# Kernel tuning notes

Hardware: AMD Instinct MI355X
Metric: run time of the kernel (lower is better)

The kernel has to match this reference:

```python
import jax, jax.numpy as jnp
import numpy as np

HEADS = 8
LN_EPS = 1e-5
BN_EPS = 1e-5
MIN_EPS, MAX_EPS = 1e-4, 10.0


def _ln(x, g, b):
    m = x.mean(-1, keepdims=True)
    v = x.var(-1, keepdims=True)
    return (x - m) / jnp.sqrt(v + LN_EPS) * g + b


def _pos2d(a, b, dim, temperature=10000.0):
    # faithful to build_2d_sincos_position_embedding(w=a, h=b)
    grid_a = jnp.arange(a, dtype=jnp.float32)
    grid_b = jnp.arange(b, dtype=jnp.float32)
    ga, gb = jnp.meshgrid(grid_a, grid_b, indexing='ij')  # (a, b)
    pos_dim = dim // 4
    omega = 1.0 / (temperature ** (jnp.arange(pos_dim, dtype=jnp.float32) / pos_dim))
    out_a = ga.flatten()[:, None] * omega[None]
    out_b = gb.flatten()[:, None] * omega[None]
    return jnp.concatenate([jnp.sin(out_a), jnp.cos(out_a), jnp.sin(out_b), jnp.cos(out_b)], axis=1)  # (a*b, dim)


def _avgpool(x, k):
    bb, cc, H, W = x.shape
    return x.reshape(bb, cc, H // k, k, W // k, k).mean((3, 5))


def setup_inputs() -> dict:
    key = jax.random.key(0)
    c1, c2, bs = 256, 512, 16
    ks = jax.random.split(key, 12)

    def lin(k, o, i):
        return (jax.random.normal(k, (o, i), jnp.float32) * (1.0 / np.sqrt(i))).astype(jnp.float32)

    return {
        'a3': jax.random.normal(ks[0], (bs, c1, 80, 80), jnp.float32),
        'a4': jax.random.normal(ks[1], (bs, c2, 40, 40), jnp.float32),
        'conv_w': lin(ks[2], c1, c2), 'conv_b': jnp.zeros((c1,), jnp.float32),
        'bn_g': jnp.ones((c1,), jnp.float32), 'bn_b': jnp.zeros((c1,), jnp.float32),
        'q_w': lin(ks[3], c1, c1), 'q_b': jnp.zeros((c1,), jnp.float32),
        'q_ln_g': jnp.ones((c1,), jnp.float32), 'q_ln_b': jnp.zeros((c1,), jnp.float32),
        'k_w': lin(ks[4], c1, c1), 'k_b': jnp.zeros((c1,), jnp.float32),
        'k_ln_g': jnp.ones((c1,), jnp.float32), 'k_ln_b': jnp.zeros((c1,), jnp.float32),
        'v_w': lin(ks[5], c1, c1), 'v_b': jnp.zeros((c1,), jnp.float32),
        'out_w': lin(ks[6], c1, c1), 'out_b': jnp.zeros((c1,), jnp.float32),
        'lin1_w': lin(ks[7], 4 * c1, c1), 'lin1_b': jnp.zeros((4 * c1,), jnp.float32),
        'lin2_w': lin(ks[8], c1, 4 * c1), 'lin2_b': jnp.zeros((c1,), jnp.float32),
        'norm1_g': jnp.ones((c1,), jnp.float32), 'norm1_b': jnp.zeros((c1,), jnp.float32),
        'norm2_g': jnp.ones((c1,), jnp.float32), 'norm2_b': jnp.zeros((c1,), jnp.float32),
        'idx': 10,
    }


def reference(a3, a4, conv_w, conv_b, bn_g, bn_b, q_w, q_b, q_ln_g, q_ln_b,
              k_w, k_b, k_ln_g, k_ln_b, v_w, v_b, out_w, out_b,
              lin1_w, lin1_b, lin2_w, lin2_b, norm1_g, norm1_b, norm2_g, norm2_b, idx):
    a3 = jnp.nan_to_num(a3, nan=0.0, posinf=1e4, neginf=-1e4)
    a4 = jnp.nan_to_num(a4, nan=0.0, posinf=1e4, neginf=-1e4)
    orig_a3, orig_a4 = a3, a4

    # high_to_low_embed: 1x1 conv + BatchNorm (eval: running_mean=0, running_var=1)
    a4e = jnp.einsum('bchw,oc->bohw', a4, conv_w) + conv_b[None, :, None, None]
    a4e = a4e / jnp.sqrt(1.0 + BN_EPS) * bn_g[None, :, None, None] + bn_b[None, :, None, None]

    if idx == 10:
        a3d = _avgpool(a3, 2)
    else:
        a3d = _avgpool(a3, 4)
        a4e = _avgpool(a4e, 2)

    bs, c, h, w = a3d.shape
    tgt = h * w
    src = a4e.shape[2] * a4e.shape[3]

    residual = a3d.reshape(bs, c, tgt).transpose(0, 2, 1)      # (bs, tgt, c)
    a3f = a3d.reshape(bs, c, tgt).transpose(2, 0, 1)            # (tgt, bs, c)
    a4f = a4e.reshape(bs, c, src).transpose(2, 0, 1)            # (src, bs, c)

    pos = _pos2d(h, w, c)[:, None, :]                           # (h*w, 1, c)
    a3f = a3f + pos
    a4f = a4f + pos                                             # src == tgt by construction

    Q = jax.nn.relu(_ln(a3f @ q_w.T + q_b, q_ln_g, q_ln_b))
    K = jax.nn.relu(_ln(a4f @ k_w.T + k_b, k_ln_g, k_ln_b))
    V = a4f @ v_w.T + v_b

    hd = c // HEADS
    Q = Q.reshape(tgt, bs, HEADS, hd).transpose(1, 2, 0, 3)     # (b, h, tgt, hd)
    K = K.reshape(src, bs, HEADS, hd).transpose(1, 2, 0, 3)
    V = V.reshape(src, bs, HEADS, hd).transpose(1, 2, 0, 3)

    m = max(src, tgt)
    wi = (np.pi / 2) * jnp.arange(1, m + 1, dtype=jnp.float32) / m  # (m,)
    sq = jnp.sin(wi[:tgt])[None, None, :, None]
    cq = jnp.cos(wi[:tgt])[None, None, :, None]
    sk = jnp.sin(wi[:src])[None, None, :, None]
    ck = jnp.cos(wi[:src])[None, None, :, None]
    Q_ = jnp.concatenate([Q * sq, Q * cq], -1)                  # (b, h, tgt, 2hd)
    K_ = jnp.concatenate([K * sk, K * ck], -1)                  # (b, h, src, 2hd)

    KV = jnp.einsum('bhsd,bhse->bhde', K_, V)                   # (b, h, 2hd, hd)
    Zden = jnp.einsum('bhld,bhd->bhl', Q_, K_.sum(2))
    Z = 1.0 / jnp.clip(Zden, MIN_EPS, MAX_EPS)
    attn = jnp.einsum('bhld,bhde->bhle', Q_, KV) * Z[..., None]  # (b, h, tgt, hd)

    attn = attn.transpose(2, 0, 1, 3).reshape(tgt, bs, c)
    out = (attn @ out_w.T + out_b).transpose(1, 0, 2)           # (bs, tgt, c)
    out = _ln(out, norm1_g, norm1_b)
    out = residual + out

    res2 = out
    ff = jax.nn.gelu(out @ lin1_w.T + lin1_b, approximate=False) @ lin2_w.T + lin2_b
    ff = _ln(ff, norm2_g, norm2_b)
    out = res2 + ff

    a3_sa = out.transpose(0, 2, 1).reshape(bs, c, h, w)
    a3_sa = jax.image.resize(a3_sa, orig_a3.shape, 'bilinear')  # align_corners=False
    a3_sa = a3_sa * orig_a3

    B4, C4, H4, W4 = orig_a4.shape
    a4_up = jax.image.resize(orig_a4, (B4, C4, 2 * H4, 2 * W4), 'bilinear')
    return (a3_sa, a4_up)
```

## Files before the change

### kernel.cpp

```cpp
#include <hip/hip_runtime.h>
#include <math.h>


typedef __attribute__((ext_vector_type(8))) short bf16x8;
typedef __attribute__((ext_vector_type(8))) unsigned short us8;
typedef __attribute__((ext_vector_type(4))) unsigned short us4h;
typedef __attribute__((ext_vector_type(4))) float f32x4;

__device__ __forceinline__ unsigned short f2bf(float f) {
  unsigned int u = __float_as_uint(f);
  u += 0x7fff + ((u >> 16) & 1);
  return (unsigned short)(u >> 16);
}
__device__ __forceinline__ float bf2f(unsigned short u) {
  return __uint_as_float(((unsigned int)u) << 16);
}

__device__ __forceinline__ void gload16(const void* g, void* l) {
  __builtin_amdgcn_global_load_lds(
      (const __attribute__((address_space(1))) void*)g,
      (__attribute__((address_space(3))) void*)l, 16, 0, 0);
}

__global__ __launch_bounds__(256) void wprep_kernel(
    const float* __restrict__ cw, const float* __restrict__ qw,
    const float* __restrict__ kw, const float* __restrict__ vw,
    const float* __restrict__ ow, const float* __restrict__ l1w,
    const float* __restrict__ l2w, unsigned short* __restrict__ wbf) {
  int gid = blockIdx.x * 256 + threadIdx.x;
  size_t e0 = (size_t)gid * 8;
  const float* src; size_t off;
  if (e0 < 131072)      { src = cw;  off = e0; }
  else if (e0 < 196608) { src = qw;  off = e0 - 131072; }
  else if (e0 < 262144) { src = kw;  off = e0 - 196608; }
  else if (e0 < 327680) { src = vw;  off = e0 - 262144; }
  else if (e0 < 393216) { src = ow;  off = e0 - 327680; }
  else if (e0 < 655360) { src = l1w; off = e0 - 393216; }
  else                  { src = l2w; off = e0 - 655360; }
  float4 v0 = *(const float4*)(src + off);
  float4 v1 = *(const float4*)(src + off + 4);
  us8 r;
  r[0] = f2bf(v0.x); r[1] = f2bf(v0.y); r[2] = f2bf(v0.z); r[3] = f2bf(v0.w);
  r[4] = f2bf(v1.x); r[5] = f2bf(v1.y); r[6] = f2bf(v1.z); r[7] = f2bf(v1.w);
  *(us8*)(wbf + e0) = r;
}

__global__ void pos_kernel(float* __restrict__ pos) {
  int s = blockIdx.x, c = threadIdx.x;
  int y = s / 40, x = s - y * 40;
  int quad = c >> 6, i = c & 63;
  float omega = expf(-(float)i * (9.2103403719761836f / 64.0f));
  float coord = (quad < 2) ? (float)y : (float)x;
  float a = coord * omega;
  pos[s * 256 + c] = (quad & 1) ? cosf(a) : sinf(a);
}

__global__ __launch_bounds__(640) void avgpool_kernel(
    const float* __restrict__ a3, const float* __restrict__ pos,
    unsigned short* __restrict__ X3) {
  __shared__ float buf2[256][44];
  int y = blockIdx.x, b = blockIdx.y;
  int tid = threadIdx.x;
  int x2 = tid % 20, cq = tid / 20;
#pragma unroll
  for (int it = 0; it < 8; ++it) {
    int c = cq + 32 * it;
    const float* p = a3 + (((size_t)(b * 256 + c) * 80 + 2 * y) * 80 + x2 * 4);
    float4 r0 = *(const float4*)p;
    float4 r1 = *(const float4*)(p + 80);
    buf2[c][2 * x2]     = 0.25f * ((r0.x + r0.y) + (r1.x + r1.y));
    buf2[c][2 * x2 + 1] = 0.25f * ((r0.z + r0.w) + (r1.z + r1.w));
  }
  __syncthreads();
  size_t t0 = (size_t)b * 1600 + y * 40;
  int sbase = y * 40;
#pragma unroll
  for (int it = 0; it < 4; ++it) {
    int idx = it * 640 + tid;
    int c = idx & 255, xq = idx >> 8;
    int x0 = xq * 4;
    float4 v = *(const float4*)&buf2[c][x0];
#pragma unroll
    for (int j = 0; j < 4; ++j) {
      float pv = pos[(size_t)(sbase + x0 + j) * 256 + c];
      float vv = (j == 0) ? v.x : (j == 1) ? v.y : (j == 2) ? v.z : v.w;
      X3[(t0 + x0 + j) * 256 + c] = f2bf(vv + pv);
    }
  }
}

__global__ __launch_bounds__(256) void a4t_kernel(
    const float* __restrict__ a4, unsigned short* __restrict__ a4t) {
  __shared__ float buf[64][65];
  int s0 = blockIdx.x * 64, k0 = blockIdx.y * 64, b = blockIdx.z;
  const float* src = a4 + ((size_t)b * 512 + k0) * 1600 + s0;
#pragma unroll
  for (int p = 0; p < 4; ++p) {
    int idx = p * 256 + threadIdx.x;
    int kk = idx >> 4, s4 = (idx & 15) * 4;
    float4 v = *(const float4*)(src + (size_t)kk * 1600 + s4);
    buf[kk][s4 + 0] = v.x; buf[kk][s4 + 1] = v.y;
    buf[kk][s4 + 2] = v.z; buf[kk][s4 + 3] = v.w;
  }
  __syncthreads();
  unsigned short* dst = a4t + ((size_t)b * 1600 + s0) * 512 + k0;
#pragma unroll
  for (int p = 0; p < 4; ++p) {
    int idx = p * 256 + threadIdx.x;
    int ss = idx >> 4, kq = (idx & 15) * 4;
    us4h v;
    v[0] = f2bf(buf[kq + 0][ss]); v[1] = f2bf(buf[kq + 1][ss]);
    v[2] = f2bf(buf[kq + 2][ss]); v[3] = f2bf(buf[kq + 3][ss]);
    *(us4h*)(dst + (size_t)ss * 512 + kq) = v;
  }
}

struct __align__(16) SmemT {
  unsigned short Albs[64][32];
  unsigned short Wlds[256][32];
  float part[4][64][2];
};

template<int EPI>
__device__ __forceinline__ void gemm_body(
    SmemT& S,
    const unsigned short* __restrict__ A, const unsigned short* __restrict__ W,
    const float* __restrict__ bias, void* __restrict__ outp,
    const int K, const int ldN, int t0, int o0,
    const float* __restrict__ posb,
    const float* __restrict__ g1, const float* __restrict__ b1,
    const unsigned short* __restrict__ res) {
  int tid = threadIdx.x;
  int lane = tid & 63, w = tid >> 6;
  int g = lane >> 4, cl = lane & 15;
  int n0 = w * 64;
  f32x4 acc[4][4] = {};

  int arow = lane >> 2, acol = (lane & 3) * 8;
  const unsigned short* ag  = A + (size_t)(t0 + w * 16 + arow) * K + acol;
  const unsigned short* wg0 = W + (size_t)(o0 + (w)      * 16 + arow) * K + acol;
  const unsigned short* wg1 = W + (size_t)(o0 + (4 + w)  * 16 + arow) * K + acol;
  const unsigned short* wg2 = W + (size_t)(o0 + (8 + w)  * 16 + arow) * K + acol;
  const unsigned short* wg3 = W + (size_t)(o0 + (12 + w) * 16 + arow) * K + acol;
  unsigned short* al  = &S.Albs[w * 16][0];
  unsigned short* wl0 = &S.Wlds[(w) * 16][0];
  unsigned short* wl1 = &S.Wlds[(4 + w) * 16][0];
  unsigned short* wl2 = &S.Wlds[(8 + w) * 16][0];
  unsigned short* wl3 = &S.Wlds[(12 + w) * 16][0];

  for (int k0 = 0; k0 < K; k0 += 32) {
    __syncthreads();
    gload16(ag + k0, al);
    gload16(wg0 + k0, wl0);
    gload16(wg1 + k0, wl1);
    gload16(wg2 + k0, wl2);
    gload16(wg3 + k0, wl3);
    __syncthreads();
    bf16x8 af[4], bw[4];
#pragma unroll
    for (int ms = 0; ms < 4; ++ms)
      af[ms] = *(const bf16x8*)&S.Albs[ms * 16 + cl][g * 8];
#pragma unroll
    for (int ns = 0; ns < 4; ++ns)
      bw[ns] = *(const bf16x8*)&S.Wlds[n0 + ns * 16 + cl][g * 8];
#pragma unroll
    for (int ms = 0; ms < 4; ++ms)
#pragma unroll
      for (int ns = 0; ns < 4; ++ns)
        acc[ms][ns] = __builtin_amdgcn_mfma_f32_16x16x32_bf16(af[ms], bw[ns], acc[ms][ns], 0, 0, 0);
  }

  float bv[4];
#pragma unroll
  for (int ns = 0; ns < 4; ++ns) bv[ns] = bias[o0 + n0 + ns * 16 + cl];
  int sbase = t0 % 1600;

  if constexpr (EPI == 2 || EPI == 3 || EPI == 5) {
#pragma unroll
    for (int ms = 0; ms < 4; ++ms) {
#pragma unroll
      for (int i = 0; i < 4; ++i) {
        float p = 0.f, q = 0.f;
#pragma unroll
        for (int ns = 0; ns < 4; ++ns) {
          float v = acc[ms][ns][i] + bv[ns];
          p += v; q += v * v;
        }
        p += __shfl_xor(p, 1); q += __shfl_xor(q, 1);
        p += __shfl_xor(p, 2); q += __shfl_xor(q, 2);
        p += __shfl_xor(p, 4); q += __shfl_xor(q, 4);
        p += __shfl_xor(p, 8); q += __shfl_xor(q, 8);
        if (cl == 0) {
          int rl = ms * 16 + g * 4 + i;
          S.part[w][rl][0] = p;
          S.part[w][rl][1] = q;
        }
      }
    }
    __syncthreads();
  }

  if constexpr (EPI == 5) {
    float* of = (float*)outp;
    int bb = t0 / 1600;
#pragma unroll
    for (int ms = 0; ms < 4; ++ms) {
      int rl0 = ms * 16 + g * 4;
      float mean[4], inv[4];
#pragma unroll
      for (int i = 0; i < 4; ++i) {
        float sp = (S.part[0][rl0 + i][0] + S.part[1][rl0 + i][0]) +
                   (S.part[2][rl0 + i][0] + S.part[3][rl0 + i][0]);
        float sq = (S.part[0][rl0 + i][1] + S.part[1][rl0 + i][1]) +
                   (S.part[2][rl0 + i][1] + S.part[3][rl0 + i][1]);
        mean[i] = sp * (1.f / 256.f);
        float var = sq * (1.f / 256.f) - mean[i] * mean[i];
        inv[i] = rsqrtf(var + 1e-5f);
      }
#pragma unroll
      for (int ns = 0; ns < 4; ++ns) {
        int col = n0 + ns * 16 + cl;
        float gg = g1[col], b2 = b1[col];
        float4 y;
#pragma unroll
        for (int i = 0; i < 4; ++i) {
          float v = acc[ms][ns][i] + bv[ns];
          float yy = (v - mean[i]) * inv[i] * gg + b2;
          yy += bf2f(res[(size_t)(t0 + rl0 + i) * 256 + col]);
          if (i == 0) y.x = yy; else if (i == 1) y.y = yy;
          else if (i == 2) y.z = yy; else y.w = yy;
        }
        *(float4*)(of + ((size_t)(bb * 256 + col) * 1600) + sbase + rl0) = y;
      }
    }
    return;
  }

  unsigned short* ob = (unsigned short*)outp;
#pragma unroll
  for (int ms = 0; ms < 4; ++ms) {
#pragma unroll
    for (int i = 0; i < 4; ++i) {
      int rl = ms * 16 + g * 4 + i;
      int t = t0 + rl;
      float mean = 0.f, inv = 0.f;
      if constexpr (EPI == 2 || EPI == 3) {
        float sp = (S.part[0][rl][0] + S.part[1][rl][0]) + (S.part[2][rl][0] + S.part[3][rl][0]);
        float sq = (S.part[0][rl][1] + S.part[1][rl][1]) + (S.part[2][rl][1] + S.part[3][rl][1]);
        mean = sp * (1.f / 256.f);
        float var = sq * (1.f / 256.f) - mean * mean;
        inv = rsqrtf(var + 1e-5f);
      }
#pragma unroll
      for (int ns = 0; ns < 4; ++ns) {
        int col = n0 + ns * 16 + cl;
        float v = acc[ms][ns][i] + bv[ns];
        size_t oidx = (size_t)t * ldN + o0 + col;
        if constexpr (EPI == 0) {
          ob[oidx] = f2bf(v);
        } else if constexpr (EPI == 1) {
          const float is = 0.99999500003749968f;
          float y = v * (is * g1[col]) + b1[col] + posb[(size_t)(sbase + rl) * 256 + col];
          ob[oidx] = f2bf(y);
        } else if constexpr (EPI == 2) {
          float y = (v - mean) * inv * g1[col] + b1[col];
          ob[oidx] = f2bf(fmaxf(y, 0.f));
        } else if constexpr (EPI == 3) {
          float y = (v - mean) * inv * g1[col] + b1[col];
          y += bf2f(res[(size_t)t * 256 + col]) - posb[(size_t)(sbase + rl) * 256 + col];
          ob[oidx] = f2bf(y);
        } else if constexpr (EPI == 4) {
          float y = 0.5f * v * (1.f + erff(v * 0.7071067811865475f));
          ob[oidx] = f2bf(y);
        }
      }
    }
  }
}

template<int EPI>
__global__ __launch_bounds__(256) void fgemm(
    const unsigned short* __restrict__ A, const unsigned short* __restrict__ W,
    const float* __restrict__ bias, void* __restrict__ outp,
    const int K, const int ldN,
    const float* __restrict__ posb,
    const float* __restrict__ g1, const float* __restrict__ b1,
    const unsigned short* __restrict__ res) {
  __shared__ SmemT S;
  gemm_body<EPI>(S, A, W, bias, outp, K, ldN, blockIdx.x * 64, blockIdx.y * 256,
                 posb, g1, b1, res);
}

__global__ __launch_bounds__(256) void qkv_kernel(
    const unsigned short* __restrict__ X3b, const unsigned short* __restrict__ X4b,
    const unsigned short* __restrict__ w_q, const unsigned short* __restrict__ w_k,
    const unsigned short* __restrict__ w_v,
    const float* __restrict__ q_b, const float* __restrict__ k_b, const float* __restrict__ v_b,
    const float* __restrict__ q_g, const float* __restrict__ q_bt,
    const float* __restrict__ k_g, const float* __restrict__ k_bt,
    unsigned short* __restrict__ Qo, unsigned short* __restrict__ Ko,
    unsigned short* __restrict__ Vo) {
  __shared__ SmemT S;
  int t0 = blockIdx.x * 64;
  if (blockIdx.y == 0) {
    gemm_body<2>(S, X3b, w_q, q_b, Qo, 256, 256, t0, 0, nullptr, q_g, q_bt, nullptr);
  } else if (blockIdx.y == 1) {
    gemm_body<2>(S, X4b, w_k, k_b, Ko, 256, 256, t0, 0, nullptr, k_g, k_bt, nullptr);
  } else {
    gemm_body<0>(S, X4b, w_v, v_b, Vo, 256, 256, t0, 0, nullptr, nullptr, nullptr, nullptr);
  }
}

__global__ __launch_bounds__(256) void kv_kernel(
    const unsigned short* __restrict__ Kb, const unsigned short* __restrict__ Vb,
    float* __restrict__ KVp, float* __restrict__ Ksp) {
  __shared__ float Kc[64][32];
  __shared__ float Vc[64][32];
  __shared__ float sv[64], cv[64];
  __shared__ float red[4][64];
  int bx = blockIdx.x;
  int bh = bx / 5, sp = bx - bh * 5;
  int b = bh >> 3, h = bh & 7;
  int tid = threadIdx.x;
  int e = tid & 31, dg = tid >> 5;
  int d4 = dg * 4;
  int dks = tid & 63, partid = tid >> 6;
  float accs[4] = {0.f, 0.f, 0.f, 0.f};
  float accc[4] = {0.f, 0.f, 0.f, 0.f};
  float ks = 0.f;
  size_t base = ((size_t)b * 1600) * 256 + h * 32;
  for (int s0 = sp * 320; s0 < sp * 320 + 320; s0 += 64) {
    __syncthreads();
#pragma unroll
    for (int p = 0; p < 8; ++p) {
      int si = dg + p * 8;
      Kc[si][e] = bf2f(Kb[base + (size_t)(s0 + si) * 256 + e]);
      Vc[si][e] = bf2f(Vb[base + (size_t)(s0 + si) * 256 + e]);
    }
    if (tid < 64) {
      float wv = 1.5707963267948966f * (float)(s0 + tid + 1) * (1.0f / 1600.0f);
      sv[tid] = sinf(wv);
      cv[tid] = cosf(wv);
    }
    __syncthreads();
#pragma unroll 8
    for (int si = 0; si < 64; ++si) {
      float vv = Vc[si][e];
      float sn = sv[si], cs = cv[si];
      float4 k4 = *(const float4*)&Kc[si][d4];
      float p0 = k4.x * vv, p1 = k4.y * vv, p2 = k4.z * vv, p3 = k4.w * vv;
      accs[0] = fmaf(p0, sn, accs[0]); accc[0] = fmaf(p0, cs, accc[0]);
      accs[1] = fmaf(p1, sn, accs[1]); accc[1] = fmaf(p1, cs, accc[1]);
      accs[2] = fmaf(p2, sn, accs[2]); accc[2] = fmaf(p2, cs, accc[2]);
      accs[3] = fmaf(p3, sn, accs[3]); accc[3] = fmaf(p3, cs, accc[3]);
    }
#pragma unroll 4
    for (int q = 0; q < 16; ++q) {
      int si = partid * 16 + q;
      float kvv = (dks < 32) ? Kc[si][dks] * sv[si] : Kc[si][dks - 32] * cv[si];
      ks += kvv;
    }
  }
  red[partid][dks] = ks;
  __syncthreads();
  size_t ob = (size_t)sp * 128 + bh;
  if (tid < 64)
    Ksp[ob * 64 + tid] = (red[0][tid] + red[1][tid]) + (red[2][tid] + red[3][tid]);
#pragma unroll
  for (int i = 0; i < 4; ++i) {
    KVp[ob * 2048 + (d4 + i) * 32 + e] = accs[i];
    KVp[ob * 2048 + (32 + d4 + i) * 32 + e] = accc[i];
  }
}

__global__ __launch_bounds__(256) void kvred_kernel(
    const float* __restrict__ KVp, const float* __restrict__ Ksp,
    float* __restrict__ KV, float* __restrict__ Ks) {
  int bh = blockIdx.x, tid = threadIdx.x;
  size_t o = (size_t)bh * 2048 + tid * 8;
  float4 s0 = make_float4(0, 0, 0, 0), s1 = make_float4(0, 0, 0, 0);
#pragma unroll
  for (int sp = 0; sp < 5; ++sp) {
    const float* p = KVp + ((size_t)sp * 128 + bh) * 2048 + tid * 8;
    float4 a = *(const float4*)p;
    float4 b2 = *(const float4*)(p + 4);
    s0.x += a.x; s0.y += a.y; s0.z += a.z; s0.w += a.w;
    s1.x += b2.x; s1.y += b2.y; s1.z += b2.z; s1.w += b2.w;
  }
  *(float4*)(KV + o) = s0;
  *(float4*)(KV + o + 4) = s1;
  if (tid < 64) {
    float t = 0.f;
#pragma unroll
    for (int sp = 0; sp < 5; ++sp) t += Ksp[((size_t)sp * 128 + bh) * 64 + tid];
    Ks[bh * 64 + tid] = t;
  }
}

__global__ __launch_bounds__(256) void attn_kernel(
    const unsigned short* __restrict__ Qb, const float* __restrict__ KV,
    const float* __restrict__ Ksum, unsigned short* __restrict__ attn) {
  int grp = threadIdx.x >> 5;
  int e = threadIdx.x & 31;
  int t = blockIdx.x * 8 + grp;
  int b = t / 1600, s = t - b * 1600;
  float wv = 1.5707963267948966f * (float)(s + 1) * (1.0f / 1600.0f);
  float sq = sinf(wv), cq = cosf(wv);
  const unsigned short* qrow = Qb + (size_t)t * 256;
  for (int h = 0; h < 8; ++h) {
    int bh = b * 8 + h;
    const float* kv = KV + (size_t)bh * 2048;
    const float* ksm = Ksum + (size_t)bh * 64;
    float qe = bf2f(qrow[h * 32 + e]);
    float zp = qe * (sq * ksm[e] + cq * ksm[32 + e]);
    zp += __shfl_xor(zp, 1); zp += __shfl_xor(zp, 2);
    zp += __shfl_xor(zp, 4); zp += __shfl_xor(zp, 8); zp += __shfl_xor(zp, 16);
    float acc = 0.f;
#pragma unroll 8
    for (int d = 0; d < 32; ++d) {
      float qv = bf2f(qrow[h * 32 + d]);
      acc = fmaf(qv * sq, kv[d * 32 + e], acc);
      acc = fmaf(qv * cq, kv[(32 + d) * 32 + e], acc);
    }
    float zc = fminf(fmaxf(zp, 1e-4f), 10.0f);
    attn[(size_t)t * 256 + h * 32 + e] = f2bf(acc * (1.0f / zc));
  }
}

__device__ __forceinline__ float4 up_row4(const float* sm, int Y, int q) {
  float fy = Y * 0.5f - 0.25f;
  int iy = (int)floorf(fy);
  float dy = fy - (float)iy;
  int y0 = iy < 0 ? 0 : iy;
  int y1 = (iy + 1) > 39 ? 39 : (iy + 1);
  const float* r0 = sm + y0 * 40;
  const float* r1 = sm + y1 * 40;
  int cm1 = (2 * q - 1) < 0 ? 0 : (2 * q - 1);
  int cp2 = (2 * q + 2) > 39 ? 39 : (2 * q + 2);
  float w1 = 1.f - dy;
  float s0 = w1 * r0[cm1]       + dy * r1[cm1];
  float s1 = w1 * r0[2 * q]     + dy * r1[2 * q];
  float s2 = w1 * r0[2 * q + 1] + dy * r1[2 * q + 1];
  float s3 = w1 * r0[cp2]       + dy * r1[cp2];
  float4 o;
  o.x = 0.25f * s0 + 0.75f * s1;
  o.y = 0.75f * s1 + 0.25f * s2;
  o.z = 0.25f * s1 + 0.75f * s2;
  o.w = 0.75f * s2 + 0.25f * s3;
  return o;
}

__global__ __launch_bounds__(256) void upsample_fused_kernel(
    const float* __restrict__ a3p, const float* __restrict__ a3,
    const float* __restrict__ a4, float* __restrict__ out0,
    float* __restrict__ out1) {
  __shared__ float sm[1600];
  int id = blockIdx.x;
  const float* src;
  float* outp;
  const float* mul = nullptr;
  if (id < 4096) {
    int c = id & 255, b = id >> 8;
    src = a3p + ((size_t)b * 256 + c) * 1600;
    outp = out0 + ((size_t)b * 256 + c) * 6400;
    mul = a3 + ((size_t)b * 256 + c) * 6400;
  } else {
    int id2 = id - 4096;
    int c = id2 & 511, b = id2 >> 9;
    src = a4 + ((size_t)b * 512 + c) * 1600;
    outp = out1 + ((size_t)b * 512 + c) * 6400;
  }
  for (int i = threadIdx.x; i < 400; i += 256)
    *(float4*)&sm[i * 4] = *(const float4*)(src + i * 4);
  __syncthreads();
  if (mul) {
    for (int i = threadIdx.x; i < 1600; i += 256) {
      int Y = i / 20, q = i - Y * 20;
      float4 o = up_row4(sm, Y, q);
      float4 m = *(const float4*)(mul + i * 4);
      o.x *= m.x; o.y *= m.y; o.z *= m.z; o.w *= m.w;
      *(float4*)(outp + i * 4) = o;
    }
  } else {
    for (int i = threadIdx.x; i < 1600; i += 256) {
      int Y = i / 20, q = i - Y * 20;
      float4 o = up_row4(sm, Y, q);
      *(float4*)(outp + i * 4) = o;
    }
  }
}

extern "C" void kernel_launch(void* const* d_in, const int* in_sizes, int n_in,
                              void* d_out, int out_size, void* d_ws, size_t ws_size,
                              hipStream_t stream) {
  const float* a3     = (const float*)d_in[0];
  const float* a4     = (const float*)d_in[1];
  const float* conv_w = (const float*)d_in[2];
  const float* conv_b = (const float*)d_in[3];
  const float* bn_g   = (const float*)d_in[4];
  const float* bn_b   = (const float*)d_in[5];
  const float* q_w    = (const float*)d_in[6];
  const float* q_b    = (const float*)d_in[7];
  const float* q_ln_g = (const float*)d_in[8];
  const float* q_ln_b = (const float*)d_in[9];
  const float* k_w    = (const float*)d_in[10];
  const float* k_b    = (const float*)d_in[11];
  const float* k_ln_g = (const float*)d_in[12];
  const float* k_ln_b = (const float*)d_in[13];
  const float* v_w    = (const float*)d_in[14];
  const float* v_b    = (const float*)d_in[15];
  const float* out_w  = (const float*)d_in[16];
  const float* out_b  = (const float*)d_in[17];
  const float* lin1_w = (const float*)d_in[18];
  const float* lin1_b = (const float*)d_in[19];
  const float* lin2_w = (const float*)d_in[20];
  const float* lin2_b = (const float*)d_in[21];
  const float* n1_g   = (const float*)d_in[22];
  const float* n1_b   = (const float*)d_in[23];
  const float* n2_g   = (const float*)d_in[24];
  const float* n2_b   = (const float*)d_in[25];
  (void)in_sizes; (void)n_in; (void)out_size; (void)ws_size;

  float* ws = (float*)d_ws;
  float* pos  = ws + 0;
  unsigned short* wbf = (unsigned short*)(ws + 409600);
  float* KV   = ws + 868352;
  float* Ks   = ws + 1130496;
  float* KVp  = ws + 1138688;
  float* Ksp  = ws + 2449408;
  unsigned short* X3b  = (unsigned short*)(ws + 2490368);
  unsigned short* X4b  = (unsigned short*)(ws + 5767168);
  unsigned short* Qbb  = (unsigned short*)(ws + 9043968);
  unsigned short* Kbb  = (unsigned short*)(ws + 12320768);
  unsigned short* Vbb  = (unsigned short*)(ws + 15597568);
  unsigned short* o1b  = (unsigned short*)(ws + 18874368);
  unsigned short* a4tb = (unsigned short*)(ws + 22151168);
  unsigned short* ffhb = (unsigned short*)(ws + 22151168);
  float* a3p  = ws + 9043968;

  const unsigned short* w_conv = wbf;
  const unsigned short* w_q    = wbf + 131072;
  const unsigned short* w_k    = wbf + 196608;
  const unsigned short* w_v    = wbf + 262144;
  const unsigned short* w_o    = wbf + 327680;
  const unsigned short* w_l1   = wbf + 393216;
  const unsigned short* w_l2   = wbf + 655360;

  float* out0 = (float*)d_out;
  float* out1f = out0 + (size_t)16 * 256 * 80 * 80;

  wprep_kernel<<<448, 256, 0, stream>>>(conv_w, q_w, k_w, v_w, out_w, lin1_w, lin2_w, wbf);
  pos_kernel<<<1600, 256, 0, stream>>>(pos);
  avgpool_kernel<<<dim3(40, 16), 640, 0, stream>>>(a3, pos, X3b);
  a4t_kernel<<<dim3(25, 8, 16), 256, 0, stream>>>(a4, a4tb);
  fgemm<1><<<dim3(400, 1), 256, 0, stream>>>(a4tb, w_conv, conv_b, X4b, 512, 256, pos, bn_g, bn_b, nullptr);
  qkv_kernel<<<dim3(400, 3), 256, 0, stream>>>(X3b, X4b, w_q, w_k, w_v,
      q_b, k_b, v_b, q_ln_g, q_ln_b, k_ln_g, k_ln_b, Qbb, Kbb, Vbb);
  kv_kernel<<<640, 256, 0, stream>>>(Kbb, Vbb, KVp, Ksp);
  kvred_kernel<<<128, 256, 0, stream>>>(KVp, Ksp, KV, Ks);
  attn_kernel<<<3200, 256, 0, stream>>>(Qbb, KV, Ks, Kbb );
  fgemm<3><<<dim3(400, 1), 256, 0, stream>>>(Kbb, w_o, out_b, o1b, 256, 256, pos, n1_g, n1_b, X3b);
  fgemm<4><<<dim3(400, 4), 256, 0, stream>>>(o1b, w_l1, lin1_b, ffhb, 256, 1024, nullptr, nullptr, nullptr, nullptr);
  fgemm<5><<<dim3(400, 1), 256, 0, stream>>>(ffhb, w_l2, lin2_b, a3p, 1024, 256, nullptr, n2_g, n2_b, o1b);
  upsample_fused_kernel<<<12288, 256, 0, stream>>>(a3p, a3, a4, out0, out1f);
}
```

Before: 417.2 us.

## Use 8-wave GEMM blocks with 2x4 warp tiling and merge prep kernels

The shared GEMM body now runs 8 waves per block instead of 4. Waves form a 2x4 grid, each computing a 32x64 subtile rather than 64x256/4, which halves per-wave accumulators and shares the LDS loading across more waves. The aim is more latency hiding and lower register pressure per wave, at the cost of larger blocks and more barrier participants. The weight-conversion and positional-embedding kernels are merged into one launch to save a kernel launch.

```diff
diff --git a/kernel.cpp b/kernel.cpp
--- a/kernel.cpp
+++ b/kernel.cpp
@@ -22,37 +22,38 @@
       (__attribute__((address_space(3))) void*)l, 16, 0, 0);
 }
 
-__global__ __launch_bounds__(256) void wprep_kernel(
+__global__ __launch_bounds__(256) void prep_kernel(
     const float* __restrict__ cw, const float* __restrict__ qw,
     const float* __restrict__ kw, const float* __restrict__ vw,
     const float* __restrict__ ow, const float* __restrict__ l1w,
-    const float* __restrict__ l2w, unsigned short* __restrict__ wbf) {
-  int gid = blockIdx.x * 256 + threadIdx.x;
-  size_t e0 = (size_t)gid * 8;
-  const float* src; size_t off;
-  if (e0 < 131072)      { src = cw;  off = e0; }
-  else if (e0 < 196608) { src = qw;  off = e0 - 131072; }
-  else if (e0 < 262144) { src = kw;  off = e0 - 196608; }
-  else if (e0 < 327680) { src = vw;  off = e0 - 262144; }
-  else if (e0 < 393216) { src = ow;  off = e0 - 327680; }
-  else if (e0 < 655360) { src = l1w; off = e0 - 393216; }
-  else                  { src = l2w; off = e0 - 655360; }
-  float4 v0 = *(const float4*)(src + off);
-  float4 v1 = *(const float4*)(src + off + 4);
-  us8 r;
-  r[0] = f2bf(v0.x); r[1] = f2bf(v0.y); r[2] = f2bf(v0.z); r[3] = f2bf(v0.w);
-  r[4] = f2bf(v1.x); r[5] = f2bf(v1.y); r[6] = f2bf(v1.z); r[7] = f2bf(v1.w);
-  *(us8*)(wbf + e0) = r;
-}
-
-__global__ void pos_kernel(float* __restrict__ pos) {
-  int s = blockIdx.x, c = threadIdx.x;
-  int y = s / 40, x = s - y * 40;
-  int quad = c >> 6, i = c & 63;
-  float omega = expf(-(float)i * (9.2103403719761836f / 64.0f));
-  float coord = (quad < 2) ? (float)y : (float)x;
-  float a = coord * omega;
-  pos[s * 256 + c] = (quad & 1) ? cosf(a) : sinf(a);
+    const float* __restrict__ l2w, unsigned short* __restrict__ wbf,
+    float* __restrict__ pos) {
+  if (blockIdx.x < 448) {
+    int gid = blockIdx.x * 256 + threadIdx.x;
+    size_t e0 = (size_t)gid * 8;
+    const float* src; size_t off;
+    if (e0 < 131072)      { src = cw;  off = e0; }
+    else if (e0 < 196608) { src = qw;  off = e0 - 131072; }
+    else if (e0 < 262144) { src = kw;  off = e0 - 196608; }
+    else if (e0 < 327680) { src = vw;  off = e0 - 262144; }
+    else if (e0 < 393216) { src = ow;  off = e0 - 327680; }
+    else if (e0 < 655360) { src = l1w; off = e0 - 393216; }
+    else                  { src = l2w; off = e0 - 655360; }
+    float4 v0 = *(const float4*)(src + off);
+    float4 v1 = *(const float4*)(src + off + 4);
+    us8 r;
+    r[0] = f2bf(v0.x); r[1] = f2bf(v0.y); r[2] = f2bf(v0.z); r[3] = f2bf(v0.w);
+    r[4] = f2bf(v1.x); r[5] = f2bf(v1.y); r[6] = f2bf(v1.z); r[7] = f2bf(v1.w);
+    *(us8*)(wbf + e0) = r;
+  } else {
+    int s = blockIdx.x - 448, c = threadIdx.x;
+    int y = s / 40, x = s - y * 40;
+    int quad = c >> 6, i = c & 63;
+    float omega = expf(-(float)i * (9.2103403719761836f / 64.0f));
+    float coord = (quad < 2) ? (float)y : (float)x;
+    float a = coord * omega;
+    pos[s * 256 + c] = (quad & 1) ? cosf(a) : sinf(a);
+  }
 }
 
 __global__ __launch_bounds__(640) void avgpool_kernel(
@@ -132,39 +133,33 @@
     const unsigned short* __restrict__ res) {
   int tid = threadIdx.x;
   int lane = tid & 63, w = tid >> 6;
+  int mw = w >> 2, nw = w & 3;
   int g = lane >> 4, cl = lane & 15;
-  int n0 = w * 64;
-  f32x4 acc[4][4] = {};
+  f32x4 acc[2][4] = {};
 
   int arow = lane >> 2, acol = (lane & 3) * 8;
-  const unsigned short* ag  = A + (size_t)(t0 + w * 16 + arow) * K + acol;
-  const unsigned short* wg0 = W + (size_t)(o0 + (w)      * 16 + arow) * K + acol;
-  const unsigned short* wg1 = W + (size_t)(o0 + (4 + w)  * 16 + arow) * K + acol;
-  const unsigned short* wg2 = W + (size_t)(o0 + (8 + w)  * 16 + arow) * K + acol;
-  const unsigned short* wg3 = W + (size_t)(o0 + (12 + w) * 16 + arow) * K + acol;
-  unsigned short* al  = &S.Albs[w * 16][0];
-  unsigned short* wl0 = &S.Wlds[(w) * 16][0];
-  unsigned short* wl1 = &S.Wlds[(4 + w) * 16][0];
-  unsigned short* wl2 = &S.Wlds[(8 + w) * 16][0];
-  unsigned short* wl3 = &S.Wlds[(12 + w) * 16][0];
+  const unsigned short* ag  = A + (size_t)(t0 + (w & 3) * 16 + arow) * K + acol;
+  const unsigned short* wgA = W + (size_t)(o0 + w * 16 + arow) * K + acol;
+  const unsigned short* wgB = W + (size_t)(o0 + 128 + w * 16 + arow) * K + acol;
+  unsigned short* al  = &S.Albs[(w & 3) * 16][0];
+  unsigned short* wlA = &S.Wlds[w * 16][0];
+  unsigned short* wlB = &S.Wlds[128 + w * 16][0];
 
   for (int k0 = 0; k0 < K; k0 += 32) {
     __syncthreads();
-    gload16(ag + k0, al);
-    gload16(wg0 + k0, wl0);
-    gload16(wg1 + k0, wl1);
-    gload16(wg2 + k0, wl2);
-    gload16(wg3 + k0, wl3);
+    if (w < 4) gload16(ag + k0, al);
+    gload16(wgA + k0, wlA);
+    gload16(wgB + k0, wlB);
     __syncthreads();
-    bf16x8 af[4], bw[4];
-#pragma unroll
-    for (int ms = 0; ms < 4; ++ms)
-      af[ms] = *(const bf16x8*)&S.Albs[ms * 16 + cl][g * 8];
+    bf16x8 af[2], bw[4];
+#pragma unroll
+    for (int ms = 0; ms < 2; ++ms)
+      af[ms] = *(const bf16x8*)&S.Albs[mw * 32 + ms * 16 + cl][g * 8];
 #pragma unroll
     for (int ns = 0; ns < 4; ++ns)
-      bw[ns] = *(const bf16x8*)&S.Wlds[n0 + ns * 16 + cl][g * 8];
-#pragma unroll
-    for (int ms = 0; ms < 4; ++ms)
+      bw[ns] = *(const bf16x8*)&S.Wlds[nw * 64 + ns * 16 + cl][g * 8];
+#pragma unroll
+    for (int ms = 0; ms < 2; ++ms)
 #pragma unroll
       for (int ns = 0; ns < 4; ++ns)
         acc[ms][ns] = __builtin_amdgcn_mfma_f32_16x16x32_bf16(af[ms], bw[ns], acc[ms][ns], 0, 0, 0);
@@ -172,12 +167,12 @@
 
   float bv[4];
 #pragma unroll
-  for (int ns = 0; ns < 4; ++ns) bv[ns] = bias[o0 + n0 + ns * 16 + cl];
+  for (int ns = 0; ns < 4; ++ns) bv[ns] = bias[o0 + nw * 64 + ns * 16 + cl];
   int sbase = t0 % 1600;
 
   if constexpr (EPI == 2 || EPI == 3 || EPI == 5) {
 #pragma unroll
-    for (int ms = 0; ms < 4; ++ms) {
+    for (int ms = 0; ms < 2; ++ms) {
 #pragma unroll
       for (int i = 0; i < 4; ++i) {
         float p = 0.f, q = 0.f;
@@ -191,9 +186,9 @@
         p += __shfl_xor(p, 4); q += __shfl_xor(q, 4);
         p += __shfl_xor(p, 8); q += __shfl_xor(q, 8);
         if (cl == 0) {
-          int rl = ms * 16 + g * 4 + i;
-          S.part[w][rl][0] = p;
-          S.part[w][rl][1] = q;
+          int rl = mw * 32 + ms * 16 + g * 4 + i;
+          S.part[nw][rl][0] = p;
+          S.part[nw][rl][1] = q;
         }
       }
     }
@@ -204,8 +199,8 @@
     float* of = (float*)outp;
     int bb = t0 / 1600;
 #pragma unroll
-    for (int ms = 0; ms < 4; ++ms) {
-      int rl0 = ms * 16 + g * 4;
+    for (int ms = 0; ms < 2; ++ms) {
+      int rl0 = mw * 32 + ms * 16 + g * 4;
       float mean[4], inv[4];
 #pragma unroll
       for (int i = 0; i < 4; ++i) {
@@ -219,7 +214,7 @@
       }
 #pragma unroll
       for (int ns = 0; ns < 4; ++ns) {
-        int col = n0 + ns * 16 + cl;
+        int col = nw * 64 + ns * 16 + cl;
         float gg = g1[col], b2 = b1[col];
         float4 y;
 #pragma unroll
@@ -238,10 +233,10 @@
 
   unsigned short* ob = (unsigned short*)outp;
 #pragma unroll
-  for (int ms = 0; ms < 4; ++ms) {
+  for (int ms = 0; ms < 2; ++ms) {
 #pragma unroll
     for (int i = 0; i < 4; ++i) {
-      int rl = ms * 16 + g * 4 + i;
+      int rl = mw * 32 + ms * 16 + g * 4 + i;
       int t = t0 + rl;
       float mean = 0.f, inv = 0.f;
       if constexpr (EPI == 2 || EPI == 3) {
@@ -253,7 +248,7 @@
       }
 #pragma unroll
       for (int ns = 0; ns < 4; ++ns) {
-        int col = n0 + ns * 16 + cl;
+        int col = nw * 64 + ns * 16 + cl;
         float v = acc[ms][ns][i] + bv[ns];
         size_t oidx = (size_t)t * ldN + o0 + col;
         if constexpr (EPI == 0) {
@@ -279,7 +274,7 @@
 }
 
 template<int EPI>
-__global__ __launch_bounds__(256) void fgemm(
+__global__ __launch_bounds__(512) void fgemm(
     const unsigned short* __restrict__ A, const unsigned short* __restrict__ W,
     const float* __restrict__ bias, void* __restrict__ outp,
     const int K, const int ldN,
@@ -291,7 +286,7 @@
                  posb, g1, b1, res);
 }
 
-__global__ __launch_bounds__(256) void qkv_kernel(
+__global__ __launch_bounds__(512) void qkv_kernel(
     const unsigned short* __restrict__ X3b, const unsigned short* __restrict__ X4b,
     const unsigned short* __restrict__ w_q, const unsigned short* __restrict__ w_k,
     const unsigned short* __restrict__ w_v,
@@ -549,18 +544,17 @@
   float* out0 = (float*)d_out;
   float* out1f = out0 + (size_t)16 * 256 * 80 * 80;
 
-  wprep_kernel<<<448, 256, 0, stream>>>(conv_w, q_w, k_w, v_w, out_w, lin1_w, lin2_w, wbf);
-  pos_kernel<<<1600, 256, 0, stream>>>(pos);
+  prep_kernel<<<2048, 256, 0, stream>>>(conv_w, q_w, k_w, v_w, out_w, lin1_w, lin2_w, wbf, pos);
   avgpool_kernel<<<dim3(40, 16), 640, 0, stream>>>(a3, pos, X3b);
   a4t_kernel<<<dim3(25, 8, 16), 256, 0, stream>>>(a4, a4tb);
-  fgemm<1><<<dim3(400, 1), 256, 0, stream>>>(a4tb, w_conv, conv_b, X4b, 512, 256, pos, bn_g, bn_b, nullptr);
-  qkv_kernel<<<dim3(400, 3), 256, 0, stream>>>(X3b, X4b, w_q, w_k, w_v,
+  fgemm<1><<<dim3(400, 1), 512, 0, stream>>>(a4tb, w_conv, conv_b, X4b, 512, 256, pos, bn_g, bn_b, nullptr);
+  qkv_kernel<<<dim3(400, 3), 512, 0, stream>>>(X3b, X4b, w_q, w_k, w_v,
       q_b, k_b, v_b, q_ln_g, q_ln_b, k_ln_g, k_ln_b, Qbb, Kbb, Vbb);
   kv_kernel<<<640, 256, 0, stream>>>(Kbb, Vbb, KVp, Ksp);
   kvred_kernel<<<128, 256, 0, stream>>>(KVp, Ksp, KV, Ks);
   attn_kernel<<<3200, 256, 0, stream>>>(Qbb, KV, Ks, Kbb );
-  fgemm<3><<<dim3(400, 1), 256, 0, stream>>>(Kbb, w_o, out_b, o1b, 256, 256, pos, n1_g, n1_b, X3b);
-  fgemm<4><<<dim3(400, 4), 256, 0, stream>>>(o1b, w_l1, lin1_b, ffhb, 256, 1024, nullptr, nullptr, nullptr, nullptr);
-  fgemm<5><<<dim3(400, 1), 256, 0, stream>>>(ffhb, w_l2, lin2_b, a3p, 1024, 256, nullptr, n2_g, n2_b, o1b);
+  fgemm<3><<<dim3(400, 1), 512, 0, stream>>>(Kbb, w_o, out_b, o1b, 256, 256, pos, n1_g, n1_b, X3b);
+  fgemm<4><<<dim3(400, 4), 512, 0, stream>>>(o1b, w_l1, lin1_b, ffhb, 256, 1024, nullptr, nullptr, nullptr, nullptr);
+  fgemm<5><<<dim3(400, 1), 512, 0, stream>>>(ffhb, w_l2, lin2_b, a3p, 1024, 256, nullptr, n2_g, n2_b, o1b);
   upsample_fused_kernel<<<12288, 256, 0, stream>>>(a3p, a3, a4, out0, out1f);
 }
```

New measurement: 385.6 us. 1.08x faster.
